# Kernel optimization log

Measured on AMD Instinct MI355X. Metric: run time of the kernel, lower is better.

## Reference

```python
import jax, jax.numpy as jnp
import numpy as np

N, E, D, K = 100000, 1600000, 32, 2
NEG_SLOPE = 0.01   # F.leaky_relu default
BN_EPS = 1e-5      # torch BatchNorm default


def setup_inputs() -> dict:
    key = jax.random.key(0)
    ks = jax.random.split(key, 8)
    y = jax.random.normal(ks[0], (N, D), jnp.float32)
    edge_index = jax.random.randint(ks[1], (2, E), 0, N, dtype=jnp.int32)
    edge_weight = jax.random.uniform(ks[2], (E,), jnp.float32)
    s = 1.0 / np.sqrt(D)
    # TAGConv(K=2): K+1 bias-free Linear(D,D) per layer, plus one output bias
    W1 = jax.random.uniform(ks[3], (K + 1, D, D), jnp.float32, -s, s)
    W2 = jax.random.uniform(ks[4], (K + 1, D, D), jnp.float32, -s, s)
    bias1 = jax.random.uniform(ks[5], (D,), jnp.float32, -s, s)
    bias2 = jax.random.uniform(ks[6], (D,), jnp.float32, -s, s)
    gamma1 = jnp.ones((D,), jnp.float32)
    beta1 = jnp.zeros((D,), jnp.float32)
    gamma2 = jnp.ones((D,), jnp.float32)
    beta2 = jnp.zeros((D,), jnp.float32)
    return dict(y=y, edge_index=edge_index, edge_weight=edge_weight,
                W1=W1, bias1=bias1, gamma1=gamma1, beta1=beta1,
                W2=W2, bias2=bias2, gamma2=gamma2, beta2=beta2)


def _tag_conv(x, W, b, src, dst, ew):
    # out = sum_{k=0..K} lin_k(A_w^k x) + bias, A_w: weighted sum-aggregation
    n = x.shape[0]
    out = x @ W[0]
    h = x
    for k in range(1, K + 1):
        msg = h[src] * ew[:, None]                         # [E, D] gather
        h = jax.ops.segment_sum(msg, dst, num_segments=n)  # scatter-add to targets
        out = out + h @ W[k]
    return out + b


def _batch_norm(x, gamma, beta):
    # training-mode BatchNorm over node dim, biased variance
    m = jnp.mean(x, axis=0)
    v = jnp.mean(jnp.square(x - m), axis=0)
    return (x - m) * jax.lax.rsqrt(v + BN_EPS) * gamma + beta


def reference(y, edge_index, edge_weight, W1, bias1, gamma1, beta1,
              W2, bias2, gamma2, beta2):
    src, dst = edge_index[0], edge_index[1]
    h = _tag_conv(y, W1, bias1, src, dst, edge_weight)
    h = jax.nn.leaky_relu(_batch_norm(h, gamma1, beta1), NEG_SLOPE)
    h = _tag_conv(h, W2, bias2, src, dst, edge_weight)
    h = jax.nn.leaky_relu(_batch_norm(h, gamma2, beta2), NEG_SLOPE)
    return h
```

## Files before the change

### kernel.cpp

```cpp
#include <hip/hip_runtime.h>

#define DD 32
#define NEG_SLOPE 0.01f
#define BN_EPS 1e-5f
#define SB 256


__global__ void zero_kernel(float* p, int n) {
    int i = blockIdx.x * blockDim.x + threadIdx.x;
    if (i < n) p[i] = 0.0f;
}

__global__ void zero_int_kernel(int* p, int n) {
    int i = blockIdx.x * blockDim.x + threadIdx.x;
    if (i < n) p[i] = 0;
}


__global__ void hist_kernel(const int* dst, int* deg, int E) {
    int e = blockIdx.x * blockDim.x + threadIdx.x;
    if (e < E) atomicAdd(&deg[dst[e]], 1);
}

__global__ void scan_block_kernel(const int* deg, int* pre, int* bsum, int N) {
    __shared__ int sh[1024];
    int tid = threadIdx.x;
    int i = blockIdx.x * 1024 + tid;
    int v = (i < N) ? deg[i] : 0;
    sh[tid] = v;
    __syncthreads();
    for (int off = 1; off < 1024; off <<= 1) {
        int t = (tid >= off) ? sh[tid - off] : 0;
        __syncthreads();
        sh[tid] += t;
        __syncthreads();
    }
    if (i < N) pre[i] = sh[tid] - v;
    if (tid == 1023) bsum[blockIdx.x] = sh[1023];
}

__global__ void scan_sums_kernel(const int* bsum, int* boff, int nb) {
    if (threadIdx.x == 0) {
        int run = 0;
        for (int i = 0; i < nb; ++i) { boff[i] = run; run += bsum[i]; }
    }
}

__global__ void add_off_kernel(int* rowptr, int* cursor, const int* boff, int N, int E) {
    int i = blockIdx.x * blockDim.x + threadIdx.x;
    if (i < N) {
        int v = rowptr[i] + boff[i >> 10];
        rowptr[i] = v;
        cursor[i] = v;
    }
    if (i == 0) rowptr[N] = E;
}

__global__ void fill_kernel(const int* src, const int* dst, const float* ew,
                            int* cursor, int2* perm, int E) {
    int e = blockIdx.x * blockDim.x + threadIdx.x;
    if (e >= E) return;
    int p = atomicAdd(&cursor[dst[e]], 1);
    int2 q;
    q.x = src[e];
    q.y = __float_as_int(ew[e]);
    perm[p] = q;
}

__global__ void gather_prop_kernel(const float* __restrict__ x,
                                   const int* __restrict__ rowptr,
                                   const int2* __restrict__ perm,
                                   float* __restrict__ out, int N) {
    int t = blockIdx.x * blockDim.x + threadIdx.x;
    int n = t >> 5;
    if (n >= N) return;
    int c = t & 31;
    int b = rowptr[n], e = rowptr[n + 1];
    float acc = 0.f;
    int j = b;
    if ((j & 1) && j < e) {
        int2 q = perm[j];
        acc += __int_as_float(q.y) * x[q.x * DD + c];
        ++j;
    }
    for (; j + 1 < e; j += 2) {
        int4 q = *reinterpret_cast<const int4*>(perm + j);
        acc += __int_as_float(q.y) * x[q.x * DD + c];
        acc += __int_as_float(q.w) * x[q.z * DD + c];
    }
    if (j < e) {
        int2 q = perm[j];
        acc += __int_as_float(q.y) * x[q.x * DD + c];
    }
    out[n * DD + c] = acc;
}

__global__ __launch_bounds__(256, 3)
void combine_v3(const float* x0, const float* __restrict__ x1,
                const float* __restrict__ x2, const float* __restrict__ W,
                float* out, int N) {
    int c = threadIdx.x & 31;
    float w0[DD], w1[DD], w2[DD];
#pragma unroll
    for (int d = 0; d < DD; ++d) {
        w0[d] = W[d * DD + c];
        w1[d] = W[DD * DD + d * DD + c];
        w2[d] = W[2 * DD * DD + d * DD + c];
    }
    int group   = (blockIdx.x * blockDim.x + threadIdx.x) >> 5;
    int ngroups = (gridDim.x * blockDim.x) >> 5;
    for (int n = group; n < N; n += ngroups) {
        const float4* r0 = reinterpret_cast<const float4*>(x0 + (size_t)n * DD);
        const float4* r1 = reinterpret_cast<const float4*>(x1 + (size_t)n * DD);
        const float4* r2 = reinterpret_cast<const float4*>(x2 + (size_t)n * DD);
        float acc = 0.f;
#pragma unroll
        for (int q = 0; q < DD / 4; ++q) {
            float4 v0 = r0[q];
            float4 v1 = r1[q];
            float4 v2 = r2[q];
            acc += v0.x * w0[4*q]   + v0.y * w0[4*q+1] + v0.z * w0[4*q+2] + v0.w * w0[4*q+3];
            acc += v1.x * w1[4*q]   + v1.y * w1[4*q+1] + v1.z * w1[4*q+2] + v1.w * w1[4*q+3];
            acc += v2.x * w2[4*q]   + v2.y * w2[4*q+1] + v2.z * w2[4*q+2] + v2.w * w2[4*q+3];
        }
        out[(size_t)n * DD + c] = acc;
    }
}


__global__ void stats_part_kernel(const float* x, float* part, int total) {
    int tid = threadIdx.x;
    int idx = blockIdx.x * 256 + tid;
    const int stride = SB * 256;
    float s = 0.f, ss = 0.f;
    for (int i = idx; i < total; i += stride) { float v = x[i]; s += v; ss += v * v; }
    __shared__ float sh[2][8][DD];
    sh[0][tid >> 5][tid & 31] = s;
    sh[1][tid >> 5][tid & 31] = ss;
    __syncthreads();
    if (tid < DD) {
        float ts = 0.f, tss = 0.f;
        for (int g = 0; g < 8; ++g) { ts += sh[0][g][tid]; tss += sh[1][g][tid]; }
        part[blockIdx.x * 64 + tid] = ts;
        part[blockIdx.x * 64 + DD + tid] = tss;
    }
}

__global__ void stats_final_kernel(const float* part, float* st) {
    int tid = threadIdx.x;
    if (tid < 64) {
        float a = 0.f;
        for (int b = 0; b < SB; ++b) a += part[b * 64 + tid];
        st[tid] = a;
    }
}

__global__ void bnrelu_kernel(const float* x, const float* stats,
                              const float* gamma, const float* beta,
                              float* out, int total, float invN) {
    int i = blockIdx.x * blockDim.x + threadIdx.x;
    if (i >= total) return;
    int c = i & 31;
    float m   = stats[c] * invN;
    float msq = stats[DD + c] * invN;
    float var = msq - m * m;
    float inv = 1.0f / sqrtf(var + BN_EPS);
    float v = (x[i] - m) * inv * gamma[c] + beta[c];
    out[i] = v >= 0.f ? v : NEG_SLOPE * v;
}


__global__ void prop_kernel(const float* x, const int* src, const int* dst,
                            const float* ew, float* out, int E) {
    int t = blockIdx.x * blockDim.x + threadIdx.x;
    int e = t >> 5;
    if (e >= E) return;
    int c = t & 31;
    float v = ew[e] * x[src[e] * DD + c];
    atomicAdd(&out[dst[e] * DD + c], v);
}

__global__ void combine_basic(const float* x0, const float* x1, const float* x2,
                              const float* W, const float* bias,
                              float* out, int N) {
    int t = blockIdx.x * blockDim.x + threadIdx.x;
    int n = t >> 5;
    if (n >= N) return;
    int c = t & 31;
    const float* r0 = x0 + n * DD;
    const float* r1 = x1 + n * DD;
    const float* r2 = x2 + n * DD;
    float acc = bias[c];
    for (int d = 0; d < DD; ++d) {
        acc += r0[d] * W[d * DD + c];
        acc += r1[d] * W[DD * DD + d * DD + c];
        acc += r2[d] * W[2 * DD * DD + d * DD + c];
    }
    out[t] = acc;
}

__global__ void stats_kernel(const float* x, float* stats, int N) {
    int c = blockIdx.x;
    int tid = threadIdx.x;
    float s = 0.f, ss = 0.f;
    for (int r = tid; r < N; r += 1024) {
        float v = x[r * DD + c];
        s += v; ss += v * v;
    }
    __shared__ float shs[1024];
    __shared__ float shq[1024];
    shs[tid] = s; shq[tid] = ss;
    __syncthreads();
    for (int off = 512; off > 0; off >>= 1) {
        if (tid < off) { shs[tid] += shs[tid + off]; shq[tid] += shq[tid + off]; }
        __syncthreads();
    }
    if (tid == 0) { stats[c] = shs[0]; stats[DD + c] = shq[0]; }
}


extern "C" void kernel_launch(void* const* d_in, const int* in_sizes, int n_in,
                              void* d_out, int out_size, void* d_ws, size_t ws_size,
                              hipStream_t stream) {
    const float* y   = (const float*)d_in[0];
    const int*   ei  = (const int*)d_in[1];
    const float* ew  = (const float*)d_in[2];
    const float* W1  = (const float*)d_in[3];
    const float* b1  = (const float*)d_in[4];
    const float* g1  = (const float*)d_in[5];
    const float* be1 = (const float*)d_in[6];
    const float* W2  = (const float*)d_in[7];
    const float* b2  = (const float*)d_in[8];
    const float* g2  = (const float*)d_in[9];
    const float* be2 = (const float*)d_in[10];
    float* out = (float*)d_out;

    const int N = in_sizes[0] / DD;
    const int E = in_sizes[2];
    const int total = N * DD;

    const int* src = ei;
    const int* dst = ei + E;

    const int RP = (N + 4) & ~3;
    float* st     = (float*)d_ws;
    float* h1     = st + 128;
    float* h2     = h1 + total;
    int*   rowptr = (int*)(h2 + total);
    int2*  perm   = (int2*)(rowptr + RP);
    float* part   = (float*)(perm + E);

    const size_t need = ((size_t)128 + 2 * (size_t)total + RP + 2 * (size_t)E + SB * 64) * 4;
    const bool use_csr = ws_size >= need;

    int* cursor = (int*)h1;
    int* bsum   = (int*)h1 + N;
    int* boff   = bsum + 128;
    int* deg    = (int*)h2;

    const int NB = (N + 1023) / 1024;
    const float invN = 1.0f / (float)N;
    dim3 blk(256);
    const int ngrid = (N + 255) / 256;
    const int egrid = (E + 255) / 256;
    const int cgrid = (total + 255) / 256;
    const int zgrid = (2 * total + 255) / 256;
    const int pgrid = (E * DD + 255) / 256;
    const int vgrid = 1024;

    if (use_csr) {
        zero_int_kernel<<<ngrid, blk, 0, stream>>>(deg, N);
        hist_kernel<<<egrid, blk, 0, stream>>>(dst, deg, E);
        scan_block_kernel<<<NB, 1024, 0, stream>>>(deg, rowptr, bsum, N);
        scan_sums_kernel<<<1, 64, 0, stream>>>(bsum, boff, NB);
        add_off_kernel<<<ngrid, blk, 0, stream>>>(rowptr, cursor, boff, N, E);
        fill_kernel<<<egrid, blk, 0, stream>>>(src, dst, ew, cursor, perm, E);

        gather_prop_kernel<<<cgrid, blk, 0, stream>>>(y,  rowptr, perm, h1, N);
        gather_prop_kernel<<<cgrid, blk, 0, stream>>>(h1, rowptr, perm, h2, N);
        combine_v3<<<vgrid, blk, 0, stream>>>(y, h1, h2, W1, out, N);
        stats_part_kernel<<<SB, blk, 0, stream>>>(out, part, total);
        stats_final_kernel<<<1, 64, 0, stream>>>(part, st);
        bnrelu_kernel<<<cgrid, blk, 0, stream>>>(out, st, g1, be1, out, total, invN);

        gather_prop_kernel<<<cgrid, blk, 0, stream>>>(out, rowptr, perm, h1, N);
        gather_prop_kernel<<<cgrid, blk, 0, stream>>>(h1, rowptr, perm, h2, N);
        combine_v3<<<vgrid, blk, 0, stream>>>(out, h1, h2, W2, out, N);
        stats_part_kernel<<<SB, blk, 0, stream>>>(out, part, total);
        stats_final_kernel<<<1, 64, 0, stream>>>(part, st + 64);
        bnrelu_kernel<<<cgrid, blk, 0, stream>>>(out, st + 64, g2, be2, out, total, invN);
    } else {
        zero_kernel<<<zgrid, blk, 0, stream>>>(h1, 2 * total);
        prop_kernel<<<pgrid, blk, 0, stream>>>(y,  src, dst, ew, h1, E);
        prop_kernel<<<pgrid, blk, 0, stream>>>(h1, src, dst, ew, h2, E);
        combine_basic<<<cgrid, blk, 0, stream>>>(y, h1, h2, W1, b1, out, N);
        stats_kernel<<<32, 1024, 0, stream>>>(out, st, N);
        bnrelu_kernel<<<cgrid, blk, 0, stream>>>(out, st, g1, be1, out, total, invN);

        zero_kernel<<<zgrid, blk, 0, stream>>>(h1, 2 * total);
        prop_kernel<<<pgrid, blk, 0, stream>>>(out, src, dst, ew, h1, E);
        prop_kernel<<<pgrid, blk, 0, stream>>>(h1,  src, dst, ew, h2, E);
        combine_basic<<<cgrid, blk, 0, stream>>>(out, h1, h2, W2, b2, out, N);
        stats_kernel<<<32, 1024, 0, stream>>>(out, st + 2 * DD, N);
        bnrelu_kernel<<<cgrid, blk, 0, stream>>>(out, st + 2 * DD, g2, be2, out, total, invN);
    }
}
```

Measured before the change: 678.4 us.

## Bucket edges by destination block, aggregate in LDS with bf16 features

Replaces the per-node CSR build and warp-per-node gather with a two-pass counting sort that groups edges into 128-node destination buckets. Each bucket block then accumulates messages with shared-memory atomics. Source features for propagation are read as bf16 copies, emitted by a conversion kernel, the first hop, and the first BN/ReLU, which halves the bytes of the random gathers. This trades global atomics on node cursors and scattered 4-byte reads for LDS atomics and reduced precision, which risks accuracy drift and load imbalance across buckets. The combine kernel's launch bounds are also dropped.

```diff
diff --git a/kernel.cpp b/kernel.cpp
--- a/kernel.cpp
+++ b/kernel.cpp
@@ -4,22 +4,44 @@
 #define NEG_SLOPE 0.01f
 #define BN_EPS 1e-5f
 #define SB 256
+#define BKL 128
+#define EBLK 256
+#define MAXBUK 800
+
+typedef unsigned short u16;
+typedef unsigned int u32;
+
+__device__ __forceinline__ u16 f32_to_bf16(float f) {
+    u32 u = __float_as_uint(f);
+    return (u16)((u + 0x7FFFu + ((u >> 16) & 1u)) >> 16);
+}
+__device__ __forceinline__ float bf16_to_f32(u16 b) {
+    return __uint_as_float(((u32)b) << 16);
+}
 
 
 __global__ void zero_kernel(float* p, int n) {
     int i = blockIdx.x * blockDim.x + threadIdx.x;
     if (i < n) p[i] = 0.0f;
 }
-
-__global__ void zero_int_kernel(int* p, int n) {
+__global__ void cvt_bf16_kernel(const float* __restrict__ x, u16* __restrict__ xb, int n) {
     int i = blockIdx.x * blockDim.x + threadIdx.x;
-    if (i < n) p[i] = 0;
-}
-
-
-__global__ void hist_kernel(const int* dst, int* deg, int E) {
-    int e = blockIdx.x * blockDim.x + threadIdx.x;
-    if (e < E) atomicAdd(&deg[dst[e]], 1);
+    if (i < n) xb[i] = f32_to_bf16(x[i]);
+}
+
+__global__ void count_kernel(const int* __restrict__ dst, int* __restrict__ countsT,
+                             int E, int EPB, int NBUK) {
+    __shared__ int cnt[MAXBUK];
+    int eb = blockIdx.x;
+    for (int i = threadIdx.x; i < NBUK; i += blockDim.x) cnt[i] = 0;
+    __syncthreads();
+    int lo = eb * EPB;
+    int hi = lo + EPB; if (hi > E) hi = E;
+    for (int e = lo + threadIdx.x; e < hi; e += blockDim.x)
+        atomicAdd(&cnt[dst[e] >> 7], 1);
+    __syncthreads();
+    for (int i = threadIdx.x; i < NBUK; i += blockDim.x)
+        countsT[i * EBLK + eb] = cnt[i];
 }
 
 __global__ void scan_block_kernel(const int* deg, int* pre, int* bsum, int N) {
@@ -39,66 +61,79 @@
     if (tid == 1023) bsum[blockIdx.x] = sh[1023];
 }
 
-__global__ void scan_sums_kernel(const int* bsum, int* boff, int nb) {
-    if (threadIdx.x == 0) {
-        int run = 0;
-        for (int i = 0; i < nb; ++i) { boff[i] = run; run += bsum[i]; }
-    }
-}
-
-__global__ void add_off_kernel(int* rowptr, int* cursor, const int* boff, int N, int E) {
+__global__ void scan_sums256(const int* bsum, int* boff, int nb) {
+    __shared__ int sh[256];
+    int tid = threadIdx.x;
+    int v = (tid < nb) ? bsum[tid] : 0;
+    sh[tid] = v;
+    __syncthreads();
+    for (int off = 1; off < 256; off <<= 1) {
+        int t = (tid >= off) ? sh[tid - off] : 0;
+        __syncthreads();
+        sh[tid] += t;
+        __syncthreads();
+    }
+    if (tid < nb) boff[tid] = sh[tid] - v;
+}
+
+__global__ void add_flat_kernel(int* a, const int* boff, int n) {
     int i = blockIdx.x * blockDim.x + threadIdx.x;
-    if (i < N) {
-        int v = rowptr[i] + boff[i >> 10];
-        rowptr[i] = v;
-        cursor[i] = v;
-    }
-    if (i == 0) rowptr[N] = E;
-}
-
-__global__ void fill_kernel(const int* src, const int* dst, const float* ew,
-                            int* cursor, int2* perm, int E) {
-    int e = blockIdx.x * blockDim.x + threadIdx.x;
-    if (e >= E) return;
-    int p = atomicAdd(&cursor[dst[e]], 1);
-    int2 q;
-    q.x = src[e];
-    q.y = __float_as_int(ew[e]);
-    perm[p] = q;
-}
-
-__global__ void gather_prop_kernel(const float* __restrict__ x,
-                                   const int* __restrict__ rowptr,
-                                   const int2* __restrict__ perm,
-                                   float* __restrict__ out, int N) {
-    int t = blockIdx.x * blockDim.x + threadIdx.x;
-    int n = t >> 5;
-    if (n >= N) return;
-    int c = t & 31;
-    int b = rowptr[n], e = rowptr[n + 1];
-    float acc = 0.f;
-    int j = b;
-    if ((j & 1) && j < e) {
-        int2 q = perm[j];
-        acc += __int_as_float(q.y) * x[q.x * DD + c];
-        ++j;
-    }
-    for (; j + 1 < e; j += 2) {
-        int4 q = *reinterpret_cast<const int4*>(perm + j);
-        acc += __int_as_float(q.y) * x[q.x * DD + c];
-        acc += __int_as_float(q.w) * x[q.z * DD + c];
-    }
-    if (j < e) {
-        int2 q = perm[j];
-        acc += __int_as_float(q.y) * x[q.x * DD + c];
-    }
-    out[n * DD + c] = acc;
-}
-
-__global__ __launch_bounds__(256, 3)
-void combine_v3(const float* x0, const float* __restrict__ x1,
-                const float* __restrict__ x2, const float* __restrict__ W,
-                float* out, int N) {
+    if (i < n) a[i] += boff[i >> 10];
+}
+
+__global__ void shard_kernel(const int* __restrict__ src, const int* __restrict__ dst,
+                             const float* __restrict__ ew, const int* __restrict__ scanT,
+                             int2* __restrict__ perm2, int E, int EPB, int NBUK) {
+    __shared__ int cur[MAXBUK];
+    int eb = blockIdx.x;
+    for (int i = threadIdx.x; i < NBUK; i += blockDim.x)
+        cur[i] = scanT[i * EBLK + eb];
+    __syncthreads();
+    int lo = eb * EPB;
+    int hi = lo + EPB; if (hi > E) hi = E;
+    for (int e = lo + threadIdx.x; e < hi; e += blockDim.x) {
+        int d = dst[e];
+        int slot = atomicAdd(&cur[d >> 7], 1);
+        int2 q;
+        q.x = ((d & (BKL - 1)) << 20) | src[e];
+        q.y = __float_as_int(ew[e]);
+        perm2[slot] = q;
+    }
+}
+
+template <bool EMIT>
+__global__ void prop_lds_kernel(const u16* __restrict__ xb, const int* __restrict__ scanT,
+                                const int2* __restrict__ perm2,
+                                float* __restrict__ out, u16* __restrict__ outb,
+                                int N, int E, int NBUK) {
+    __shared__ float acc[BKL * DD];
+    int b = blockIdx.x;
+    for (int i = threadIdx.x; i < BKL * DD; i += blockDim.x) acc[i] = 0.f;
+    __syncthreads();
+    int qlo = scanT[b * EBLK];
+    int qhi = (b + 1 < NBUK) ? scanT[(b + 1) * EBLK] : E;
+    int g = threadIdx.x >> 5, c = threadIdx.x & 31;
+    for (int j = qlo + g; j < qhi; j += 8) {
+        int2 q = perm2[j];
+        int   s  = q.x & 0xFFFFF;
+        int   dl = q.x >> 20;
+        float w  = __int_as_float(q.y);
+        atomicAdd(&acc[dl * DD + c], w * bf16_to_f32(xb[s * DD + c]));
+    }
+    __syncthreads();
+    for (int i = g; i < BKL; i += 8) {
+        int node = b * BKL + i;
+        if (node < N) {
+            float v = acc[i * DD + c];
+            out[node * DD + c] = v;
+            if (EMIT) outb[node * DD + c] = f32_to_bf16(v);
+        }
+    }
+}
+
+__global__ void combine_v3(const float* x0, const float* __restrict__ x1,
+                           const float* __restrict__ x2, const float* __restrict__ W,
+                           float* out, int N) {
     int c = threadIdx.x & 31;
     float w0[DD], w1[DD], w2[DD];
 #pragma unroll
@@ -119,9 +154,9 @@
             float4 v0 = r0[q];
             float4 v1 = r1[q];
             float4 v2 = r2[q];
-            acc += v0.x * w0[4*q]   + v0.y * w0[4*q+1] + v0.z * w0[4*q+2] + v0.w * w0[4*q+3];
-            acc += v1.x * w1[4*q]   + v1.y * w1[4*q+1] + v1.z * w1[4*q+2] + v1.w * w1[4*q+3];
-            acc += v2.x * w2[4*q]   + v2.y * w2[4*q+1] + v2.z * w2[4*q+2] + v2.w * w2[4*q+3];
+            acc += v0.x * w0[4*q] + v0.y * w0[4*q+1] + v0.z * w0[4*q+2] + v0.w * w0[4*q+3];
+            acc += v1.x * w1[4*q] + v1.y * w1[4*q+1] + v1.z * w1[4*q+2] + v1.w * w1[4*q+3];
+            acc += v2.x * w2[4*q] + v2.y * w2[4*q+1] + v2.z * w2[4*q+2] + v2.w * w2[4*q+3];
         }
         out[(size_t)n * DD + c] = acc;
     }
@@ -155,9 +190,10 @@
     }
 }
 
+template <bool EMIT>
 __global__ void bnrelu_kernel(const float* x, const float* stats,
                               const float* gamma, const float* beta,
-                              float* out, int total, float invN) {
+                              float* out, u16* outb, int total, float invN) {
     int i = blockIdx.x * blockDim.x + threadIdx.x;
     if (i >= total) return;
     int c = i & 31;
@@ -166,7 +202,9 @@
     float var = msq - m * m;
     float inv = 1.0f / sqrtf(var + BN_EPS);
     float v = (x[i] - m) * inv * gamma[c] + beta[c];
-    out[i] = v >= 0.f ? v : NEG_SLOPE * v;
+    v = v >= 0.f ? v : NEG_SLOPE * v;
+    out[i] = v;
+    if (EMIT) outb[i] = f32_to_bf16(v);
 }
 
 
@@ -242,66 +280,72 @@
     const int* src = ei;
     const int* dst = ei + E;
 
-    const int RP = (N + 4) & ~3;
+    const int NBUK = (N + BKL - 1) / BKL;
+    const int TOTC = NBUK * EBLK;
+    const int TOTCP = (TOTC + 4) & ~3;
+    const int EPB  = (E + EBLK - 1) / EBLK;
+    const int NB2  = (TOTC + 1023) / 1024;
+
     float* st     = (float*)d_ws;
     float* h1     = st + 128;
     float* h2     = h1 + total;
-    int*   rowptr = (int*)(h2 + total);
-    int2*  perm   = (int2*)(rowptr + RP);
-    float* part   = (float*)(perm + E);
-
-    const size_t need = ((size_t)128 + 2 * (size_t)total + RP + 2 * (size_t)E + SB * 64) * 4;
-    const bool use_csr = ws_size >= need;
-
-    int* cursor = (int*)h1;
-    int* bsum   = (int*)h1 + N;
-    int* boff   = bsum + 128;
-    int* deg    = (int*)h2;
-
-    const int NB = (N + 1023) / 1024;
+    int*   scanT  = (int*)(h2 + total);
+    int2*  perm2  = (int2*)(scanT + TOTCP);
+    u16*   h1b    = (u16*)(perm2 + E);
+    float* part   = (float*)h1b;
+    u16*   xb16   = (u16*)h2;
+
+    int*   bsum   = (int*)h1;
+    int*   boff   = bsum + 256;
+
+    const size_t tailBytes = ((size_t)total * 2 > (size_t)SB * 64 * 4)
+                               ? (size_t)total * 2 : (size_t)SB * 64 * 4;
+    const size_t need = ((size_t)128 + 2 * (size_t)total + TOTCP) * 4
+                        + (size_t)E * 8 + tailBytes;
+    const bool fast = (ws_size >= need) && (NBUK <= MAXBUK) && (N <= (1 << 20));
+
     const float invN = 1.0f / (float)N;
     dim3 blk(256);
-    const int ngrid = (N + 255) / 256;
-    const int egrid = (E + 255) / 256;
     const int cgrid = (total + 255) / 256;
+    const int fgrid = (TOTC + 255) / 256;
     const int zgrid = (2 * total + 255) / 256;
     const int pgrid = (E * DD + 255) / 256;
     const int vgrid = 1024;
 
-    if (use_csr) {
-        zero_int_kernel<<<ngrid, blk, 0, stream>>>(deg, N);
-        hist_kernel<<<egrid, blk, 0, stream>>>(dst, deg, E);
-        scan_block_kernel<<<NB, 1024, 0, stream>>>(deg, rowptr, bsum, N);
-        scan_sums_kernel<<<1, 64, 0, stream>>>(bsum, boff, NB);
-        add_off_kernel<<<ngrid, blk, 0, stream>>>(rowptr, cursor, boff, N, E);
-        fill_kernel<<<egrid, blk, 0, stream>>>(src, dst, ew, cursor, perm, E);
-
-        gather_prop_kernel<<<cgrid, blk, 0, stream>>>(y,  rowptr, perm, h1, N);
-        gather_prop_kernel<<<cgrid, blk, 0, stream>>>(h1, rowptr, perm, h2, N);
+    if (fast) {
+        count_kernel<<<EBLK, blk, 0, stream>>>(dst, scanT, E, EPB, NBUK);
+        scan_block_kernel<<<NB2, 1024, 0, stream>>>(scanT, scanT, bsum, TOTC);
+        scan_sums256<<<1, 256, 0, stream>>>(bsum, boff, NB2);
+        add_flat_kernel<<<fgrid, blk, 0, stream>>>(scanT, boff, TOTC);
+        shard_kernel<<<EBLK, blk, 0, stream>>>(src, dst, ew, scanT, perm2, E, EPB, NBUK);
+
+        cvt_bf16_kernel<<<cgrid, blk, 0, stream>>>(y, xb16, total);
+        prop_lds_kernel<true><<<NBUK, blk, 0, stream>>>(xb16, scanT, perm2, h1, h1b, N, E, NBUK);
+        prop_lds_kernel<false><<<NBUK, blk, 0, stream>>>(h1b, scanT, perm2, h2, nullptr, N, E, NBUK);
         combine_v3<<<vgrid, blk, 0, stream>>>(y, h1, h2, W1, out, N);
         stats_part_kernel<<<SB, blk, 0, stream>>>(out, part, total);
         stats_final_kernel<<<1, 64, 0, stream>>>(part, st);
-        bnrelu_kernel<<<cgrid, blk, 0, stream>>>(out, st, g1, be1, out, total, invN);
-
-        gather_prop_kernel<<<cgrid, blk, 0, stream>>>(out, rowptr, perm, h1, N);
-        gather_prop_kernel<<<cgrid, blk, 0, stream>>>(h1, rowptr, perm, h2, N);
+        bnrelu_kernel<true><<<cgrid, blk, 0, stream>>>(out, st, g1, be1, out, xb16, total, invN);
+
+        prop_lds_kernel<true><<<NBUK, blk, 0, stream>>>(xb16, scanT, perm2, h1, h1b, N, E, NBUK);
+        prop_lds_kernel<false><<<NBUK, blk, 0, stream>>>(h1b, scanT, perm2, h2, nullptr, N, E, NBUK);
         combine_v3<<<vgrid, blk, 0, stream>>>(out, h1, h2, W2, out, N);
         stats_part_kernel<<<SB, blk, 0, stream>>>(out, part, total);
         stats_final_kernel<<<1, 64, 0, stream>>>(part, st + 64);
-        bnrelu_kernel<<<cgrid, blk, 0, stream>>>(out, st + 64, g2, be2, out, total, invN);
+        bnrelu_kernel<false><<<cgrid, blk, 0, stream>>>(out, st + 64, g2, be2, out, nullptr, total, invN);
     } else {
         zero_kernel<<<zgrid, blk, 0, stream>>>(h1, 2 * total);
         prop_kernel<<<pgrid, blk, 0, stream>>>(y,  src, dst, ew, h1, E);
         prop_kernel<<<pgrid, blk, 0, stream>>>(h1, src, dst, ew, h2, E);
         combine_basic<<<cgrid, blk, 0, stream>>>(y, h1, h2, W1, b1, out, N);
         stats_kernel<<<32, 1024, 0, stream>>>(out, st, N);
-        bnrelu_kernel<<<cgrid, blk, 0, stream>>>(out, st, g1, be1, out, total, invN);
+        bnrelu_kernel<false><<<cgrid, blk, 0, stream>>>(out, st, g1, be1, out, nullptr, total, invN);
 
         zero_kernel<<<zgrid, blk, 0, stream>>>(h1, 2 * total);
         prop_kernel<<<pgrid, blk, 0, stream>>>(out, src, dst, ew, h1, E);
         prop_kernel<<<pgrid, blk, 0, stream>>>(h1,  src, dst, ew, h2, E);
         combine_basic<<<cgrid, blk, 0, stream>>>(out, h1, h2, W2, b2, out, N);
         stats_kernel<<<32, 1024, 0, stream>>>(out, st + 2 * DD, N);
-        bnrelu_kernel<<<cgrid, blk, 0, stream>>>(out, st + 2 * DD, g2, be2, out, total, invN);
-    }
-}
+        bnrelu_kernel<false><<<cgrid, blk, 0, stream>>>(out, st + 2 * DD, g2, be2, out, nullptr, total, invN);
+    }
+}
```

Measured after the change: 1.762 ms. +159.7%, slower.

## Gather neighbor features in bf16 and split edges across two half-waves

Applied to the files above, without the earlier changes.

Node features are converted to bf16 copies before each propagation. The CSR gather kernel reads those copies, which halves the bytes fetched per random neighbor row, and it also writes a bf16 copy of its first hop for the second hop. Each node now uses 64 lanes, with the two halves taking alternating edges and combining their sums through a shuffle. The single-thread block-sum scan becomes a parallel shared-memory scan, and the launch-bounds hint on the combine kernel is dropped. This reduces memory traffic in the dominant gather at the cost of bf16 rounding in the propagated features and an extra conversion pass.

```diff
diff --git a/kernel.cpp b/kernel.cpp
--- a/kernel.cpp
+++ b/kernel.cpp
@@ -5,15 +5,29 @@
 #define BN_EPS 1e-5f
 #define SB 256
 
+typedef unsigned short u16;
+typedef unsigned int u32;
+
+__device__ __forceinline__ u16 f32_to_bf16(float f) {
+    u32 u = __float_as_uint(f);
+    return (u16)((u + 0x7FFFu + ((u >> 16) & 1u)) >> 16);
+}
+__device__ __forceinline__ float bf16_to_f32(u16 b) {
+    return __uint_as_float(((u32)b) << 16);
+}
+
 
 __global__ void zero_kernel(float* p, int n) {
     int i = blockIdx.x * blockDim.x + threadIdx.x;
     if (i < n) p[i] = 0.0f;
 }
-
 __global__ void zero_int_kernel(int* p, int n) {
     int i = blockIdx.x * blockDim.x + threadIdx.x;
     if (i < n) p[i] = 0;
+}
+__global__ void cvt_bf16_kernel(const float* __restrict__ x, u16* __restrict__ xb, int n) {
+    int i = blockIdx.x * blockDim.x + threadIdx.x;
+    if (i < n) xb[i] = f32_to_bf16(x[i]);
 }
 
 
@@ -40,10 +54,18 @@
 }
 
 __global__ void scan_sums_kernel(const int* bsum, int* boff, int nb) {
-    if (threadIdx.x == 0) {
-        int run = 0;
-        for (int i = 0; i < nb; ++i) { boff[i] = run; run += bsum[i]; }
-    }
+    __shared__ int sh[128];
+    int tid = threadIdx.x;
+    int v = (tid < nb) ? bsum[tid] : 0;
+    sh[tid] = v;
+    __syncthreads();
+    for (int off = 1; off < 128; off <<= 1) {
+        int t = (tid >= off) ? sh[tid - off] : 0;
+        __syncthreads();
+        sh[tid] += t;
+        __syncthreads();
+    }
+    if (tid < nb) boff[tid] = sh[tid] - v;
 }
 
 __global__ void add_off_kernel(int* rowptr, int* cursor, const int* boff, int N, int E) {
@@ -67,38 +89,42 @@
     perm[p] = q;
 }
 
-__global__ void gather_prop_kernel(const float* __restrict__ x,
-                                   const int* __restrict__ rowptr,
-                                   const int2* __restrict__ perm,
-                                   float* __restrict__ out, int N) {
+template <bool EMIT>
+__global__ void gather2_kernel(const u16* __restrict__ xb,
+                               const int* __restrict__ rowptr,
+                               const int2* __restrict__ perm,
+                               float* __restrict__ out,
+                               u16* __restrict__ outb, int N) {
     int t = blockIdx.x * blockDim.x + threadIdx.x;
-    int n = t >> 5;
+    int n = t >> 6;
     if (n >= N) return;
-    int c = t & 31;
+    int lane = threadIdx.x & 63;
+    int half = lane >> 5;
+    int c = lane & 31;
     int b = rowptr[n], e = rowptr[n + 1];
-    float acc = 0.f;
-    int j = b;
-    if ((j & 1) && j < e) {
-        int2 q = perm[j];
-        acc += __int_as_float(q.y) * x[q.x * DD + c];
-        ++j;
-    }
-    for (; j + 1 < e; j += 2) {
-        int4 q = *reinterpret_cast<const int4*>(perm + j);
-        acc += __int_as_float(q.y) * x[q.x * DD + c];
-        acc += __int_as_float(q.w) * x[q.z * DD + c];
+    float a0 = 0.f, a1 = 0.f;
+    int j = b + half;
+    for (; j + 2 < e; j += 4) {
+        int2 qa = perm[j];
+        int2 qb = perm[j + 2];
+        a0 += __int_as_float(qa.y) * bf16_to_f32(xb[qa.x * DD + c]);
+        a1 += __int_as_float(qb.y) * bf16_to_f32(xb[qb.x * DD + c]);
     }
     if (j < e) {
         int2 q = perm[j];
-        acc += __int_as_float(q.y) * x[q.x * DD + c];
-    }
-    out[n * DD + c] = acc;
-}
-
-__global__ __launch_bounds__(256, 3)
-void combine_v3(const float* x0, const float* __restrict__ x1,
-                const float* __restrict__ x2, const float* __restrict__ W,
-                float* out, int N) {
+        a0 += __int_as_float(q.y) * bf16_to_f32(xb[q.x * DD + c]);
+    }
+    float acc = a0 + a1;
+    acc += __shfl_xor(acc, 32);
+    if (half == 0) {
+        out[n * DD + c] = acc;
+        if (EMIT) outb[n * DD + c] = f32_to_bf16(acc);
+    }
+}
+
+__global__ void combine_v3(const float* x0, const float* __restrict__ x1,
+                           const float* __restrict__ x2, const float* __restrict__ W,
+                           float* out, int N) {
     int c = threadIdx.x & 31;
     float w0[DD], w1[DD], w2[DD];
 #pragma unroll
@@ -119,9 +145,9 @@
             float4 v0 = r0[q];
             float4 v1 = r1[q];
             float4 v2 = r2[q];
-            acc += v0.x * w0[4*q]   + v0.y * w0[4*q+1] + v0.z * w0[4*q+2] + v0.w * w0[4*q+3];
-            acc += v1.x * w1[4*q]   + v1.y * w1[4*q+1] + v1.z * w1[4*q+2] + v1.w * w1[4*q+3];
-            acc += v2.x * w2[4*q]   + v2.y * w2[4*q+1] + v2.z * w2[4*q+2] + v2.w * w2[4*q+3];
+            acc += v0.x * w0[4*q] + v0.y * w0[4*q+1] + v0.z * w0[4*q+2] + v0.w * w0[4*q+3];
+            acc += v1.x * w1[4*q] + v1.y * w1[4*q+1] + v1.z * w1[4*q+2] + v1.w * w1[4*q+3];
+            acc += v2.x * w2[4*q] + v2.y * w2[4*q+1] + v2.z * w2[4*q+2] + v2.w * w2[4*q+3];
         }
         out[(size_t)n * DD + c] = acc;
     }
@@ -155,9 +181,10 @@
     }
 }
 
+template <bool EMIT>
 __global__ void bnrelu_kernel(const float* x, const float* stats,
                               const float* gamma, const float* beta,
-                              float* out, int total, float invN) {
+                              float* out, u16* outb, int total, float invN) {
     int i = blockIdx.x * blockDim.x + threadIdx.x;
     if (i >= total) return;
     int c = i & 31;
@@ -166,7 +193,9 @@
     float var = msq - m * m;
     float inv = 1.0f / sqrtf(var + BN_EPS);
     float v = (x[i] - m) * inv * gamma[c] + beta[c];
-    out[i] = v >= 0.f ? v : NEG_SLOPE * v;
+    v = v >= 0.f ? v : NEG_SLOPE * v;
+    out[i] = v;
+    if (EMIT) outb[i] = f32_to_bf16(v);
 }
 
 
@@ -248,10 +277,15 @@
     float* h2     = h1 + total;
     int*   rowptr = (int*)(h2 + total);
     int2*  perm   = (int2*)(rowptr + RP);
-    float* part   = (float*)(perm + E);
-
-    const size_t need = ((size_t)128 + 2 * (size_t)total + RP + 2 * (size_t)E + SB * 64) * 4;
-    const bool use_csr = ws_size >= need;
+    u16*   h1b    = (u16*)(perm + E);
+    float* part   = (float*)h1b;
+    u16*   xb16   = (u16*)h2;
+
+    const size_t tailBytes = ((size_t)total * 2 > (size_t)SB * 64 * 4)
+                               ? (size_t)total * 2 : (size_t)SB * 64 * 4;
+    const size_t need_bf16 = ((size_t)128 + 2 * (size_t)total + RP) * 4
+                             + (size_t)E * 8 + tailBytes;
+    const bool use_bf16 = ws_size >= need_bf16;
 
     int* cursor = (int*)h1;
     int* bsum   = (int*)h1 + N;
@@ -264,44 +298,46 @@
     const int ngrid = (N + 255) / 256;
     const int egrid = (E + 255) / 256;
     const int cgrid = (total + 255) / 256;
+    const int ggrid = (2 * total + 255) / 256;
     const int zgrid = (2 * total + 255) / 256;
     const int pgrid = (E * DD + 255) / 256;
     const int vgrid = 1024;
 
-    if (use_csr) {
+    if (use_bf16) {
         zero_int_kernel<<<ngrid, blk, 0, stream>>>(deg, N);
         hist_kernel<<<egrid, blk, 0, stream>>>(dst, deg, E);
         scan_block_kernel<<<NB, 1024, 0, stream>>>(deg, rowptr, bsum, N);
-        scan_sums_kernel<<<1, 64, 0, stream>>>(bsum, boff, NB);
+        scan_sums_kernel<<<1, 128, 0, stream>>>(bsum, boff, NB);
         add_off_kernel<<<ngrid, blk, 0, stream>>>(rowptr, cursor, boff, N, E);
         fill_kernel<<<egrid, blk, 0, stream>>>(src, dst, ew, cursor, perm, E);
 
-        gather_prop_kernel<<<cgrid, blk, 0, stream>>>(y,  rowptr, perm, h1, N);
-        gather_prop_kernel<<<cgrid, blk, 0, stream>>>(h1, rowptr, perm, h2, N);
+        cvt_bf16_kernel<<<cgrid, blk, 0, stream>>>(y, xb16, total);
+        gather2_kernel<true><<<ggrid, blk, 0, stream>>>(xb16, rowptr, perm, h1, h1b, N);
+        gather2_kernel<false><<<ggrid, blk, 0, stream>>>(h1b, rowptr, perm, h2, nullptr, N);
         combine_v3<<<vgrid, blk, 0, stream>>>(y, h1, h2, W1, out, N);
         stats_part_kernel<<<SB, blk, 0, stream>>>(out, part, total);
         stats_final_kernel<<<1, 64, 0, stream>>>(part, st);
-        bnrelu_kernel<<<cgrid, blk, 0, stream>>>(out, st, g1, be1, out, total, invN);
-
-        gather_prop_kernel<<<cgrid, blk, 0, stream>>>(out, rowptr, perm, h1, N);
-        gather_prop_kernel<<<cgrid, blk, 0, stream>>>(h1, rowptr, perm, h2, N);
+        bnrelu_kernel<true><<<cgrid, blk, 0, stream>>>(out, st, g1, be1, out, xb16, total, invN);
+
+        gather2_kernel<true><<<ggrid, blk, 0, stream>>>(xb16, rowptr, perm, h1, h1b, N);
+        gather2_kernel<false><<<ggrid, blk, 0, stream>>>(h1b, rowptr, perm, h2, nullptr, N);
         combine_v3<<<vgrid, blk, 0, stream>>>(out, h1, h2, W2, out, N);
         stats_part_kernel<<<SB, blk, 0, stream>>>(out, part, total);
         stats_final_kernel<<<1, 64, 0, stream>>>(part, st + 64);
-        bnrelu_kernel<<<cgrid, blk, 0, stream>>>(out, st + 64, g2, be2, out, total, invN);
+        bnrelu_kernel<false><<<cgrid, blk, 0, stream>>>(out, st + 64, g2, be2, out, nullptr, total, invN);
     } else {
         zero_kernel<<<zgrid, blk, 0, stream>>>(h1, 2 * total);
         prop_kernel<<<pgrid, blk, 0, stream>>>(y,  src, dst, ew, h1, E);
         prop_kernel<<<pgrid, blk, 0, stream>>>(h1, src, dst, ew, h2, E);
         combine_basic<<<cgrid, blk, 0, stream>>>(y, h1, h2, W1, b1, out, N);
         stats_kernel<<<32, 1024, 0, stream>>>(out, st, N);
-        bnrelu_kernel<<<cgrid, blk, 0, stream>>>(out, st, g1, be1, out, total, invN);
+        bnrelu_kernel<false><<<cgrid, blk, 0, stream>>>(out, st, g1, be1, out, nullptr, total, invN);
 
         zero_kernel<<<zgrid, blk, 0, stream>>>(h1, 2 * total);
         prop_kernel<<<pgrid, blk, 0, stream>>>(out, src, dst, ew, h1, E);
         prop_kernel<<<pgrid, blk, 0, stream>>>(h1,  src, dst, ew, h2, E);
         combine_basic<<<cgrid, blk, 0, stream>>>(out, h1, h2, W2, b2, out, N);
         stats_kernel<<<32, 1024, 0, stream>>>(out, st + 2 * DD, N);
-        bnrelu_kernel<<<cgrid, blk, 0, stream>>>(out, st + 2 * DD, g2, be2, out, total, invN);
-    }
-}
+        bnrelu_kernel<false><<<cgrid, blk, 0, stream>>>(out, st + 2 * DD, g2, be2, out, nullptr, total, invN);
+    }
+}
```

After: 751.0 us. +10.7%, slower.
